# Kernel tuning notes

Hardware: AMD Instinct MI355X
Metric: run time of the kernel (lower is better)

Reference implementation:

```python
import jax, jax.numpy as jnp
import numpy as np

B, C, T = 8, 512, 8192
NQ, CBS, CBD = 9, 1024, 8
EPS = 1e-12  # F.normalize eps


def setup_inputs() -> dict:
    key = jax.random.key(0)
    ks = jax.random.split(key, 12)
    n = lambda i, shape, s: jax.random.normal(ks[i], shape, jnp.float32) * s
    return {
        "z": n(0, (B, C, T), 1.0),
        "down_w": n(1, (2, C, C, 2), 0.02),   # [layer, out, in, k] (torch Conv1d layout)
        "down_b": n(2, (2, C), 0.01),
        "up_w": n(3, (2, C, C, 2), 0.02),     # [layer, in, out, k] (torch ConvTranspose1d layout)
        "up_b": n(4, (2, C), 0.01),
        "in_v": n(5, (NQ, CBD, C), 0.05),     # weight_norm direction of in_proj 1x1 conv
        "in_g": 1.0 + n(6, (NQ, CBD), 0.02),  # weight_norm magnitude
        "in_b": n(7, (NQ, CBD), 0.01),
        "out_v": n(8, (NQ, C, CBD), 0.05),
        "out_g": 1.0 + n(9, (NQ, C), 0.02),
        "out_b": n(10, (NQ, C), 0.01),
        "codebooks": n(11, (NQ, CBS, CBD), 1.0),
    }


def _wn(g, v):
    # weight_norm (dim=0): per-output-row rescale
    return g[:, None] * v / jnp.linalg.norm(v, axis=1, keepdims=True)


def _l2norm(x):
    return x / jnp.maximum(jnp.linalg.norm(x, axis=-1, keepdims=True), EPS)


def _forward(z, down_w, down_b, up_w, up_b, in_v, in_g, in_b, out_v, out_g, out_b, codebooks):
    # --- downsample: two Conv1d(k=2, s=2) ---
    x = z
    for l in range(2):
        b, c, t = x.shape
        xr = x.reshape(b, c, t // 2, 2)
        x = jnp.einsum('bitk,oik->bot', xr, down_w[l]) + down_b[l][None, :, None]

    residual = x
    z_q = jnp.zeros_like(x)
    commit_loss = jnp.float32(0.0)
    cb_loss = jnp.float32(0.0)
    codes = []
    for i in range(NQ):
        # in_proj 1x1 conv (weight-normed)
        w_in = _wn(in_g[i], in_v[i])                 # [CBD, C]
        z_e = jnp.einsum('bdt,cd->bct', residual, w_in) + in_b[i][None, :, None]  # [B, CBD, T']
        # decode_latents: L2-normalize + squared-euclid via matmul + argmax
        bt = z_e.shape[0] * z_e.shape[2]
        enc = z_e.transpose(0, 2, 1).reshape(bt, CBD)
        enc_n = _l2norm(enc)
        cbk = codebooks[i]
        cb_n = _l2norm(cbk)
        dist = ((enc_n ** 2).sum(1, keepdims=True)
                - 2.0 * enc_n @ cb_n.T
                + (cb_n ** 2).sum(1)[None, :])        # [B*T', CBS]
        idx = jnp.argmax(-dist, axis=1).reshape(z_e.shape[0], -1)  # [B, T']
        z_q_i = cbk[idx].transpose(0, 2, 1)           # [B, CBD, T'] (un-normalized codebook rows)
        # losses (eval: mask all-true -> per-batch mean over (1,2) then batch mean == global mean)
        commit_loss = commit_loss + ((z_e - jax.lax.stop_gradient(z_q_i)) ** 2).mean()
        cb_loss = cb_loss + ((z_q_i - jax.lax.stop_gradient(z_e)) ** 2).mean()
        # straight-through + out_proj 1x1 conv (weight-normed)
        z_st = z_e + jax.lax.stop_gradient(z_q_i - z_e)
        w_out = _wn(out_g[i], out_v[i])               # [C, CBD]
        z_q_out = jnp.einsum('bct,dc->bdt', z_st, w_out) + out_b[i][None, :, None]
        z_q = z_q + z_q_out
        residual = residual - z_q_out
        codes.append(idx)
    codes = jnp.stack(codes, axis=1)                  # [B, NQ, T']

    x = z_q
    for l in range(2):
        b, c, t = x.shape
        x = jnp.einsum('bit,iok->botk', x, up_w[l]).reshape(b, C, t * 2) + up_b[l][None, :, None]
    return x, codes, commit_loss, cb_loss


def reference(z, down_w, down_b, up_w, up_b, in_v, in_g, in_b, out_v, out_g, out_b, codebooks):
    return _forward(z, down_w, down_b, up_w, up_b, in_v, in_g, in_b, out_v, out_g, out_b, codebooks)
```

## Files before the change

### kernel.cpp

```cpp
#include <hip/hip_runtime.h>
#include <math.h>


using u16 = unsigned short;
typedef __attribute__((ext_vector_type(8))) short bf16x8;
typedef __attribute__((ext_vector_type(8))) u16 su16x8;
typedef __attribute__((ext_vector_type(4))) float f32x4;

constexpr int NQ = 9, CBS = 1024, CBD = 8;
constexpr int TQ = 2048;
constexpr int NTOK = 16384;
constexpr int ASTR = 524288;
#define EPSN 1e-12f

constexpr size_t OFF_X1   = 0;
constexpr size_t OFF_U2   = 0;
constexpr size_t OFF_Q    = 14417920;
constexpr size_t OFF_E0T  = 15597568;
constexpr size_t OFF_X2   = 16777216;
constexpr size_t OFF_ZQF  = OFF_X2;
constexpr size_t OFF_DWP  = OFF_X2 + 8388608;
constexpr size_t OFF_UWP  = OFF_DWP + 1572864;
constexpr size_t OFF_WINN = OFF_UWP + 1048576;
constexpr size_t OFF_WOUT = OFF_WINN + 36864;
constexpr size_t OFF_CBS  = OFF_WOUT + 36864;
constexpr size_t OFF_PT   = OFF_CBS + 18432;
constexpr size_t OFF_BEFF = OFF_PT + 2340;
constexpr size_t OFF_BSUM = OFF_BEFF + 72;
constexpr size_t OFF_LOSS = OFF_BSUM + 512;

__global__ void prep_wp(const float* __restrict__ down_w, const float* __restrict__ up_w,
                        float* __restrict__ ws) {
  int idx = blockIdx.x * 256 + threadIdx.x;
  int mat = idx >> 19, e = idx & 524287;
  if (mat < 2) {
    float v = down_w[(size_t)mat * 524288 + e];
    u16* dst = (u16*)(ws + OFF_DWP) + (size_t)mat * 3 * ASTR;
    unsigned u = __float_as_uint(v);
    dst[e] = (u16)(u >> 16);
    float r = v - __uint_as_float(u & 0xFFFF0000u);
    unsigned ur = __float_as_uint(r);
    dst[ASTR + e] = (u16)(ur >> 16);
    float r2 = r - __uint_as_float(ur & 0xFFFF0000u);
    dst[2 * ASTR + e] = (u16)(__float_as_uint(r2) >> 16);
  } else {
    int l = mat - 2;
    int m = e >> 9, c = e & 511;
    float v = up_w[(size_t)l * 524288 + ((size_t)c * 512 + (m >> 1)) * 2 + (m & 1)];
    u16* dst = (u16*)(ws + OFF_UWP) + (size_t)l * 2 * ASTR;
    unsigned u = __float_as_uint(v);
    dst[e] = (u16)(u >> 16);
    float r = v - __uint_as_float(u & 0xFFFF0000u);
    dst[ASTR + e] = (u16)(__float_as_uint(r) >> 16);
  }
}

__global__ void prep_small1(const float* __restrict__ in_v, const float* __restrict__ in_g,
                            const float* __restrict__ out_v, const float* __restrict__ out_g,
                            const float* __restrict__ out_b, const float* __restrict__ codebooks,
                            float* __restrict__ ws) {
  int bid = blockIdx.x, tid = threadIdx.x;
  if (bid < 18) {
    int wid = bid * 4 + (tid >> 6), lane = tid & 63;
    if (wid < 72) {
      const float* v = in_v + (size_t)wid * 512;
      float ss = 0.f;
      for (int c = lane; c < 512; c += 64) ss += v[c] * v[c];
      #pragma unroll
      for (int o = 32; o; o >>= 1) ss += __shfl_xor(ss, o);
      float sc = in_g[wid] / sqrtf(ss);
      float* dst = ws + OFF_WINN + (size_t)wid * 512;
      for (int c = lane; c < 512; c += 64) dst[c] = v[c] * sc;
    }
  } else if (bid < 36) {
    int r = (bid - 18) * 256 + tid;
    if (r < 4608) {
      int i = r >> 9, c = r & 511;
      const float* v = out_v + (size_t)r * 8;
      float ss = 0.f;
      #pragma unroll
      for (int d = 0; d < 8; d++) ss += v[d] * v[d];
      float sc = out_g[r] / sqrtf(ss);
      float* dst = ws + OFF_WOUT + (size_t)c * 72 + i * 8;
      #pragma unroll
      for (int d = 0; d < 8; d++) dst[d] = v[d] * sc;
    }
  } else if (bid < 72) {
    int r = (bid - 36) * 256 + tid;
    if (r < 9216) {
      int i = r >> 10, j = r & 1023;
      const float* v = codebooks + (size_t)r * 8;
      float ss = 0.f;
      #pragma unroll
      for (int d = 0; d < 8; d++) ss += v[d] * v[d];
      float nm = fmaxf(sqrtf(ss), EPSN);
      float nsq = 0.f;
      #pragma unroll
      for (int d = 0; d < 8; d++) { float cn = v[d] / nm; nsq += cn * cn; }
      ws[OFF_CBS + ((size_t)i * 2 + 0) * 1024 + j] = 2.0f / nm;
      ws[OFF_CBS + ((size_t)i * 2 + 1) * 1024 + j] = nsq;
    }
  } else {
    int c = (bid - 72) * 256 + tid;
    if (c < 512) {
      float s = 0.f;
      #pragma unroll
      for (int j = 0; j < 9; j++) s += out_b[j * 512 + c];
      ws[OFF_BSUM + c] = s;
    }
  }
}

__global__ void prep2(const float* __restrict__ in_b, const float* __restrict__ out_b,
                      float* __restrict__ ws) {
  int gw = blockIdx.x * 4 + (threadIdx.x >> 6), lane = threadIdx.x & 63;
  const float* WinN = ws + OFF_WINN;
  const float* WoutS = ws + OFF_WOUT;
  if (gw < 2304) {
    int tri = gw >> 6, dd = gw & 63;
    int ip = 1;
    while (tri >= ip * (ip + 1) / 2) ip++;
    int i = tri - ip * (ip - 1) / 2;
    int d = dd >> 3, dp = dd & 7;
    const float* a = WinN + (size_t)(ip * 8 + d) * 512;
    float s = 0.f;
    for (int c = lane; c < 512; c += 64) s += a[c] * WoutS[(size_t)c * 72 + i * 8 + dp];
    #pragma unroll
    for (int o = 32; o; o >>= 1) s += __shfl_xor(s, o);
    if (lane == 0) ws[OFF_PT + (size_t)tri * 65 + dd] = s;
  } else if (gw < 2376) {
    int r = gw - 2304;
    int i = r >> 3;
    const float* a = WinN + (size_t)r * 512;
    float s = 0.f;
    for (int c = lane; c < 512; c += 64) {
      float ob = 0.f;
      for (int j = 0; j < i; j++) ob += out_b[j * 512 + c];
      s += a[c] * ob;
    }
    #pragma unroll
    for (int o = 32; o; o >>= 1) s += __shfl_xor(s, o);
    if (lane == 0) ws[OFF_BEFF + r] = in_b[r] - s;
  }
}

template <int NS, int GM, int EPI>
__global__ __launch_bounds__(256) void gemmT(const u16* __restrict__ Ap,
                                             const float* __restrict__ Bsrc,
                                             const float* __restrict__ bias,
                                             float* __restrict__ Out,
                                             int K, int N) {
  __shared__ u16 Bp[2][NS][128][32];
  const int tid = threadIdx.x;
  const int w = tid >> 6, l = tid & 63;
  const int g = l >> 4, li = l & 15;
  const int wr = w >> 1, wc = w & 1;
  const int n0 = blockIdx.x * 128, m0 = blockIdx.y * 128;
  const int nn = tid & 127, kw = tid >> 7;
  const int bb = (GM == 0) ? (n0 >> 12) : (n0 >> 11);
  const int tb = (GM == 0) ? ((n0 & 4095) + nn) : ((n0 & 2047) + nn);

  f32x4 acc[4][4];
  #pragma unroll
  for (int a = 0; a < 4; a++)
    #pragma unroll
    for (int b = 0; b < 4; b++) acc[a][b] = (f32x4){0.f, 0.f, 0.f, 0.f};

  float pvA[16], pvB[16];

#define LOADB(PV, K0)                                                           \
  if constexpr (GM == 0) {                                                      \
    int i0_ = ((K0) >> 1) + kw * 8;                                             \
    _Pragma("unroll")                                                           \
    for (int j2_ = 0; j2_ < 8; ++j2_)                                           \
      *(float2*)&PV[2 * j2_] =                                                  \
          *(const float2*)(Bsrc + ((size_t)(bb * 512 + i0_ + j2_) << 13) + 2 * tb); \
  } else if constexpr (GM == 1) {                                               \
    int i0_ = ((K0) >> 1) + kw * 8;                                             \
    _Pragma("unroll")                                                           \
    for (int j2_ = 0; j2_ < 8; ++j2_)                                           \
      *(float2*)&PV[2 * j2_] =                                                  \
          *(const float2*)(Bsrc + ((size_t)(i0_ + j2_) << 15) + bb * 4096 + 2 * tb); \
  } else {                                                                      \
    _Pragma("unroll")                                                           \
    for (int j_ = 0; j_ < 16; ++j_)                                             \
      PV[j_] = Bsrc[(size_t)((K0) + kw * 16 + j_) * N + n0 + nn];               \
  }

  const int sw = (nn >> 1) & 3;
  const int c0 = ((2 * kw) ^ sw) << 3, c1 = ((2 * kw + 1) ^ sw) << 3;

#define STAGE(BUF, PV)                                                          \
  {                                                                             \
    su16x8 pa_[NS], pb_[NS];                                                    \
    _Pragma("unroll")                                                           \
    for (int j_ = 0; j_ < 8; ++j_) {                                            \
      {                                                                         \
        float v_ = PV[j_];                                                      \
        unsigned u_ = __float_as_uint(v_);                                      \
        pa_[0][j_] = (u16)(u_ >> 16);                                           \
        float r_ = v_ - __uint_as_float(u_ & 0xFFFF0000u);                      \
        unsigned ur_ = __float_as_uint(r_);                                     \
        pa_[1][j_] = (u16)(ur_ >> 16);                                          \
        if constexpr (NS == 3) {                                                \
          float r2_ = r_ - __uint_as_float(ur_ & 0xFFFF0000u);                  \
          pa_[2][j_] = (u16)(__float_as_uint(r2_) >> 16);                       \
        }                                                                       \
      }                                                                         \
      {                                                                         \
        float v_ = PV[8 + j_];                                                  \
        unsigned u_ = __float_as_uint(v_);                                      \
        pb_[0][j_] = (u16)(u_ >> 16);                                           \
        float r_ = v_ - __uint_as_float(u_ & 0xFFFF0000u);                      \
        unsigned ur_ = __float_as_uint(r_);                                     \
        pb_[1][j_] = (u16)(ur_ >> 16);                                          \
        if constexpr (NS == 3) {                                                \
          float r2_ = r_ - __uint_as_float(ur_ & 0xFFFF0000u);                  \
          pb_[2][j_] = (u16)(__float_as_uint(r2_) >> 16);                       \
        }                                                                       \
      }                                                                         \
    }                                                                           \
    _Pragma("unroll")                                                           \
    for (int p_ = 0; p_ < NS; ++p_) {                                           \
      *(su16x8*)&Bp[BUF][p_][nn][c0] = pa_[p_];                                 \
      *(su16x8*)&Bp[BUF][p_][nn][c1] = pb_[p_];                                 \
    }                                                                           \
  }

#define COMPUTE(BUF, K0)                                                        \
  {                                                                             \
    bf16x8 bfr_[4][NS];                                                         \
    _Pragma("unroll")                                                           \
    for (int fn_ = 0; fn_ < 4; ++fn_) {                                         \
      int row_ = wc * 64 + fn_ * 16 + li;                                       \
      int cs_ = ((g ^ ((row_ >> 1) & 3)) << 3);                                 \
      _Pragma("unroll")                                                         \
      for (int q_ = 0; q_ < NS; ++q_)                                           \
        bfr_[fn_][q_] = *(const bf16x8*)&Bp[BUF][q_][row_][cs_];                \
    }                                                                           \
    const u16* arow_ = Ap + (size_t)(m0 + wr * 64 + li) * K + (K0) + g * 8;     \
    _Pragma("unroll")                                                           \
    for (int fm_ = 0; fm_ < 4; ++fm_) {                                         \
      bf16x8 afr_[NS];                                                          \
      _Pragma("unroll")                                                         \
      for (int p_ = 0; p_ < NS; ++p_)                                           \
        afr_[p_] = *(const bf16x8*)(arow_ + (size_t)p_ * ASTR + (size_t)fm_ * 16 * K); \
      _Pragma("unroll")                                                         \
      for (int fn_ = 0; fn_ < 4; ++fn_) {                                       \
        f32x4 a_ = acc[fm_][fn_];                                               \
        if constexpr (NS == 3) {                                                \
          a_ = __builtin_amdgcn_mfma_f32_16x16x32_bf16(afr_[2], bfr_[fn_][0], a_, 0, 0, 0); \
          a_ = __builtin_amdgcn_mfma_f32_16x16x32_bf16(afr_[1], bfr_[fn_][1], a_, 0, 0, 0); \
          a_ = __builtin_amdgcn_mfma_f32_16x16x32_bf16(afr_[0], bfr_[fn_][2], a_, 0, 0, 0); \
          a_ = __builtin_amdgcn_mfma_f32_16x16x32_bf16(afr_[1], bfr_[fn_][0], a_, 0, 0, 0); \
          a_ = __builtin_amdgcn_mfma_f32_16x16x32_bf16(afr_[0], bfr_[fn_][1], a_, 0, 0, 0); \
          a_ = __builtin_amdgcn_mfma_f32_16x16x32_bf16(afr_[0], bfr_[fn_][0], a_, 0, 0, 0); \
        } else {                                                                \
          a_ = __builtin_amdgcn_mfma_f32_16x16x32_bf16(afr_[1], bfr_[fn_][0], a_, 0, 0, 0); \
          a_ = __builtin_amdgcn_mfma_f32_16x16x32_bf16(afr_[0], bfr_[fn_][1], a_, 0, 0, 0); \
          a_ = __builtin_amdgcn_mfma_f32_16x16x32_bf16(afr_[0], bfr_[fn_][0], a_, 0, 0, 0); \
        }                                                                       \
        acc[fm_][fn_] = a_;                                                     \
      }                                                                         \
    }                                                                           \
  }

  LOADB(pvA, 0)
  LOADB(pvB, 32)
  STAGE(0, pvA)
  if (64 < K) { LOADB(pvA, 64) }
  __syncthreads();

  for (int k0 = 0; k0 < K; k0 += 64) {
    STAGE(1, pvB)
    if (k0 + 96 < K) { LOADB(pvB, k0 + 96) }
    COMPUTE(0, k0)
    __syncthreads();
    if (k0 + 64 < K) { STAGE(0, pvA) }
    if (k0 + 128 < K) { LOADB(pvA, k0 + 128) }
    COMPUTE(1, k0 + 32)
    __syncthreads();
  }
#undef LOADB
#undef STAGE
#undef COMPUTE

  const int mb = m0 + wr * 64 + g * 4;
  const int nb = n0 + wc * 64 + li;
  if constexpr (EPI == 0) {
    #pragma unroll
    for (int fn = 0; fn < 4; ++fn) {
      int n = nb + fn * 16;
      #pragma unroll
      for (int fm = 0; fm < 4; ++fm)
        #pragma unroll
        for (int r = 0; r < 4; ++r) {
          int o = mb + fm * 16 + r;
          Out[(size_t)o * 32768 + n] = acc[fm][fn][r] + bias[o];
        }
    }
  } else if constexpr (EPI == 1) {
    #pragma unroll
    for (int fn = 0; fn < 4; ++fn) {
      int n = nb + fn * 16;
      int b = n >> 11, t = n & 2047;
      #pragma unroll
      for (int fm = 0; fm < 4; ++fm)
        #pragma unroll
        for (int r = 0; r < 4; ++r) {
          int o = mb + fm * 16 + r;
          Out[((size_t)((b << 9) + o)) * 2048 + t] = acc[fm][fn][r] + bias[o];
        }
    }
  } else if constexpr (EPI == 2) {
    #pragma unroll
    for (int fn = 0; fn < 4; ++fn) {
      int n = nb + fn * 16;
      int b = n >> 11, t = n & 2047;
      #pragma unroll
      for (int fm = 0; fm < 4; ++fm)
        #pragma unroll
        for (int rp = 0; rp < 2; ++rp) {
          int m2 = mb + fm * 16 + 2 * rp;
          int o = m2 >> 1;
          float bv = bias[o];
          float2 st = make_float2(acc[fm][fn][2 * rp] + bv, acc[fm][fn][2 * rp + 1] + bv);
          *(float2*)&Out[(size_t)o * 32768 + (size_t)b * 4096 + 2 * t] = st;
        }
    }
  } else {
    #pragma unroll
    for (int fn = 0; fn < 4; ++fn) {
      int n = nb + fn * 16;
      int b = n >> 12, t1 = n & 4095;
      #pragma unroll
      for (int fm = 0; fm < 4; ++fm)
        #pragma unroll
        for (int rp = 0; rp < 2; ++rp) {
          int m2 = mb + fm * 16 + 2 * rp;
          int o = m2 >> 1;
          float bv = bias[o];
          float2 st = make_float2(acc[fm][fn][2 * rp] + bv, acc[fm][fn][2 * rp + 1] + bv);
          *(float2*)&Out[((size_t)((b << 9) + o)) * 8192 + 2 * t1] = st;
        }
    }
  }
}

template <int GATHER, int SCATTER>
__global__ __launch_bounds__(256) void gemm_conv(const float* __restrict__ A,
                                                 const float* __restrict__ Bsrc,
                                                 const float* __restrict__ bias,
                                                 float* __restrict__ Out,
                                                 int M, int K, int N, int Tt) {
  constexpr int BM = 128, BN = 128, BK = 16;
  __shared__ float As[BK][BM + 4];
  __shared__ float Bs[BK][BN + 4];
  int tid = threadIdx.x;
  int tx = tid & 15, ty = tid >> 4;
  int n0 = blockIdx.x * BN, m0 = blockIdx.y * BM;
  int b = n0 / Tt, t0 = n0 % Tt;
  float acc[8][8];
  #pragma unroll
  for (int i = 0; i < 8; i++)
    #pragma unroll
    for (int j = 0; j < 8; j++) acc[i][j] = 0.f;

  for (int k0 = 0; k0 < K; k0 += BK) {
    #pragma unroll
    for (int rep = 0; rep < 2; rep++) {
      int f = tid + rep * 256;
      int row = f >> 2, c4 = (f & 3) << 2;
      int m = m0 + row, k = k0 + c4;
      float4 v = make_float4(0.f, 0.f, 0.f, 0.f);
      if (m < M) {
        if (k + 3 < K) {
          v = *(const float4*)(A + (size_t)m * K + k);
        } else {
          float tmp[4] = {0.f, 0.f, 0.f, 0.f};
          for (int c = 0; c < 4; c++)
            if (k + c < K) tmp[c] = A[(size_t)m * K + k + c];
          v = make_float4(tmp[0], tmp[1], tmp[2], tmp[3]);
        }
      }
      As[c4 + 0][row] = v.x; As[c4 + 1][row] = v.y;
      As[c4 + 2][row] = v.z; As[c4 + 3][row] = v.w;
    }
    #pragma unroll
    for (int rep = 0; rep < 2; rep++) {
      int f = tid + rep * 256;
      int kk = f >> 5, n4 = (f & 31) << 2;
      int k = k0 + kk;
      float4 v = make_float4(0.f, 0.f, 0.f, 0.f);
      if (GATHER == 1) {
        v = *(const float4*)(Bsrc + ((size_t)(b * K + k)) * Tt + t0 + n4);
      } else {
        if (k < K) v = *(const float4*)(Bsrc + (size_t)k * N + n0 + n4);
      }
      *(float4*)&Bs[kk][n4] = v;
    }
    __syncthreads();
    #pragma unroll
    for (int kk = 0; kk < BK; kk++) {
      float a[8], bb[8];
      *(float4*)&a[0] = *(float4*)&As[kk][ty * 8];
      *(float4*)&a[4] = *(float4*)&As[kk][ty * 8 + 4];
      *(float4*)&bb[0] = *(float4*)&Bs[kk][tx * 8];
      *(float4*)&bb[4] = *(float4*)&Bs[kk][tx * 8 + 4];
      #pragma unroll
      for (int i = 0; i < 8; i++)
        #pragma unroll
        for (int j = 0; j < 8; j++) acc[i][j] = fmaf(a[i], bb[j], acc[i][j]);
    }
    __syncthreads();
  }
  if (SCATTER == 0) {
    #pragma unroll
    for (int i = 0; i < 8; i++) {
      int m = m0 + ty * 8 + i;
      if (m < M) {
        float bv = bias ? bias[m] : 0.f;
        float* p = Out + ((size_t)(b * M + m)) * Tt + t0 + tx * 8;
        *(float4*)p = make_float4(acc[i][0] + bv, acc[i][1] + bv, acc[i][2] + bv, acc[i][3] + bv);
        *(float4*)(p + 4) = make_float4(acc[i][4] + bv, acc[i][5] + bv, acc[i][6] + bv, acc[i][7] + bv);
      }
    }
  } else {
    #pragma unroll
    for (int j = 0; j < 8; j++) {
      int n = n0 + tx * 8 + j;
      int m = m0 + ty * 8;
      if (m < M) {
        float* p = Out + (size_t)n * M + m;
        if (m + 7 < M) {
          *(float4*)p = make_float4(acc[0][j], acc[1][j], acc[2][j], acc[3][j]);
          *(float4*)(p + 4) = make_float4(acc[4][j], acc[5][j], acc[6][j], acc[7][j]);
        } else {
          for (int i = 0; i < 8 && m + i < M; i++) p[i] = acc[i][j];
        }
      }
    }
  }
}

__global__ __launch_bounds__(256) void rvq_kernel(const float* __restrict__ codebooks,
                                                  const float* __restrict__ e0t,
                                                  const float* __restrict__ cbsW,
                                                  const float* __restrict__ ptW,
                                                  const float* __restrict__ beffW,
                                                  float* __restrict__ Qout,
                                                  float* __restrict__ codesOut,
                                                  float* __restrict__ lossPart) {
  __shared__ float cbv[8][1024];
  __shared__ float cbs2[2][1024];
  __shared__ float Pt[36 * 65];
  __shared__ float est[16][72];
  __shared__ float lred[4];
  int tid = threadIdx.x, wid = tid >> 6, lane = tid & 63;
  int nb0 = blockIdx.x * 16;
  for (int idx = tid; idx < 2340; idx += 256) Pt[idx] = ptW[idx];
  for (int idx = tid; idx < 16 * 72; idx += 256)
    est[idx / 72][idx % 72] = e0t[(size_t)nb0 * 72 + idx] + beffW[idx % 72];
  float lossLocal = 0.f;

  for (int i = 0; i < NQ; i++) {
    __syncthreads();
    const float* cbg = codebooks + (size_t)i * CBS * CBD;
    for (int lin = tid; lin < 2048; lin += 256) {
      int j = lin >> 1, half = (lin & 1) << 2;
      float4 v = *(const float4*)(cbg + (size_t)j * 8 + half);
      cbv[half + 0][j] = v.x; cbv[half + 1][j] = v.y;
      cbv[half + 2][j] = v.z; cbv[half + 3][j] = v.w;
    }
    for (int lin = tid; lin < 1024; lin += 256) {
      cbs2[0][lin] = cbsW[((size_t)i * 2 + 0) * 1024 + lin];
      cbs2[1][lin] = cbsW[((size_t)i * 2 + 1) * 1024 + lin];
    }
    __syncthreads();

    float ze[4][8], en[4][8];
    #pragma unroll
    for (int w = 0; w < 4; w++) {
      int tokl = wid * 4 + w;
      float ss = 0.f;
      #pragma unroll
      for (int d = 0; d < 8; d++) { float v = est[tokl][i * 8 + d]; ze[w][d] = v; ss += v * v; }
      float inv = 1.0f / fmaxf(sqrtf(ss), EPSN);
      #pragma unroll
      for (int d = 0; d < 8; d++) en[w][d] = ze[w][d] * inv;
    }
    float best[4]; int bidx[4];
    #pragma unroll
    for (int w = 0; w < 4; w++) { best[w] = -INFINITY; bidx[w] = 0; }
    #pragma unroll 4
    for (int r = 0; r < 16; r++) {
      int j = lane + (r << 6);
      float c0 = cbv[0][j], c1 = cbv[1][j], c2 = cbv[2][j], c3 = cbv[3][j];
      float c4 = cbv[4][j], c5 = cbv[5][j], c6 = cbv[6][j], c7 = cbv[7][j];
      float ti = cbs2[0][j], ns = cbs2[1][j];
      #pragma unroll
      for (int w = 0; w < 4; w++) {
        float dt = en[w][0] * c0;
        dt = fmaf(en[w][1], c1, dt); dt = fmaf(en[w][2], c2, dt);
        dt = fmaf(en[w][3], c3, dt); dt = fmaf(en[w][4], c4, dt);
        dt = fmaf(en[w][5], c5, dt); dt = fmaf(en[w][6], c6, dt);
        dt = fmaf(en[w][7], c7, dt);
        float s = fmaf(dt, ti, -ns);
        if (s > best[w]) { best[w] = s; bidx[w] = j; }
      }
    }
    #pragma unroll
    for (int w = 0; w < 4; w++) {
      #pragma unroll
      for (int off = 32; off; off >>= 1) {
        float so = __shfl_xor(best[w], off);
        int jo = __shfl_xor(bidx[w], off);
        if (so > best[w] || (so == best[w] && jo < bidx[w])) { best[w] = so; bidx[w] = jo; }
      }
    }
    int d = lane & 7;
    #pragma unroll
    for (int w = 0; w < 4; w++) {
      int jstar = bidx[w];
      int tokl = wid * 4 + w;
      int n = nb0 + tokl;
      float qd = cbv[d][jstar];
      float diff = ze[w][d] - qd;
      float sq = diff * diff;
      sq += __shfl_xor(sq, 1); sq += __shfl_xor(sq, 2); sq += __shfl_xor(sq, 4);
      if (lane == 0) lossLocal += sq;
      if (lane < 8) Qout[(size_t)(i * 8 + lane) * NTOK + n] = qd;
      if (lane == 0) codesOut[(size_t)((n >> 11) * NQ + i) * TQ + (n & (TQ - 1))] = (float)jstar;
      if (i < NQ - 1) {
        int f = lane >> 3, d2 = lane & 7;
        int ip = i + 1 + f;
        if (ip < NQ) {
          int tri = (ip * (ip - 1)) / 2 + i;
          const float* prow = &Pt[tri * 65 + d2 * 8];
          float s = 0.f;
          #pragma unroll
          for (int dp = 0; dp < 8; dp++) s = fmaf(prow[dp], cbv[dp][jstar], s);
          est[tokl][ip * 8 + d2] -= s;
        }
      }
    }
  }
  if (lane == 0) lred[wid] = lossLocal;
  __syncthreads();
  if (tid == 0) {
    float s = ((lred[0] + lred[1]) + lred[2]) + lred[3];
    lossPart[blockIdx.x] = s;
  }
}

__global__ void loss_fin(const float* __restrict__ lossPart, float* __restrict__ out) {
  __shared__ float s[256];
  int tid = threadIdx.x;
  float v = 0.f;
  for (int r = 0; r < 4; r++) v += lossPart[tid + r * 256];
  s[tid] = v;
  __syncthreads();
  for (int w = 128; w; w >>= 1) {
    if (tid < w) s[tid] += s[tid + w];
    __syncthreads();
  }
  if (tid == 0) {
    float total = s[0] / 131072.0f;
    out[0] = total;
    out[1] = total;
  }
}

extern "C" void kernel_launch(void* const* d_in, const int* in_sizes, int n_in,
                              void* d_out, int out_size, void* d_ws, size_t ws_size,
                              hipStream_t stream) {
  const float* z      = (const float*)d_in[0];
  const float* down_w = (const float*)d_in[1];
  const float* down_b = (const float*)d_in[2];
  const float* up_w   = (const float*)d_in[3];
  const float* up_b   = (const float*)d_in[4];
  const float* in_v   = (const float*)d_in[5];
  const float* in_g   = (const float*)d_in[6];
  const float* in_b   = (const float*)d_in[7];
  const float* out_v  = (const float*)d_in[8];
  const float* out_g  = (const float*)d_in[9];
  const float* out_b  = (const float*)d_in[10];
  const float* codebooks = (const float*)d_in[11];
  float* ws = (float*)d_ws;
  float* xout = (float*)d_out;
  float* codesOut = xout + (size_t)8 * 512 * 8192;
  float* lossOut = codesOut + (size_t)8 * NQ * TQ;
  const u16* dwp = (const u16*)(ws + OFF_DWP);
  const u16* uwp = (const u16*)(ws + OFF_UWP);

  hipLaunchKernelGGL(prep_wp, dim3(8192), dim3(256), 0, stream, down_w, up_w, ws);
  hipLaunchKernelGGL(prep_small1, dim3(74), dim3(256), 0, stream,
                     in_v, in_g, out_v, out_g, out_b, codebooks, ws);
  hipLaunchKernelGGL(prep2, dim3(594), dim3(256), 0, stream, in_b, out_b, ws);
  hipLaunchKernelGGL((gemmT<3, 0, 0>), dim3(256, 4), dim3(256), 0, stream,
                     dwp, z, down_b, ws + OFF_X1, 1024, 32768);
  hipLaunchKernelGGL((gemmT<3, 1, 1>), dim3(128, 4), dim3(256), 0, stream,
                     dwp + (size_t)3 * ASTR, ws + OFF_X1, down_b + 512, ws + OFF_X2, 1024, 16384);
  hipLaunchKernelGGL((gemm_conv<1, 1>), dim3(128, 1), dim3(256), 0, stream,
                     ws + OFF_WINN, ws + OFF_X2, (const float*)nullptr, ws + OFF_E0T, 72, 512, 16384, 2048);
  hipLaunchKernelGGL(rvq_kernel, dim3(1024), dim3(256), 0, stream,
                     codebooks, ws + OFF_E0T, ws + OFF_CBS, ws + OFF_PT, ws + OFF_BEFF,
                     ws + OFF_Q, codesOut, ws + OFF_LOSS);
  hipLaunchKernelGGL((gemm_conv<2, 0>), dim3(128, 4), dim3(256), 0, stream,
                     ws + OFF_WOUT, ws + OFF_Q, ws + OFF_BSUM, ws + OFF_ZQF, 512, 72, 16384, 16384);
  hipLaunchKernelGGL((gemmT<2, 2, 2>), dim3(128, 8), dim3(256), 0, stream,
                     uwp, ws + OFF_ZQF, up_b, ws + OFF_U2, 512, 16384);
  hipLaunchKernelGGL((gemmT<2, 2, 3>), dim3(256, 8), dim3(256), 0, stream,
                     uwp + (size_t)2 * ASTR, ws + OFF_U2, up_b + 512, xout, 512, 32768);
  hipLaunchKernelGGL(loss_fin, dim3(1), dim3(256), 0, stream, ws + OFF_LOSS, lossOut);
}
```

Measured before the change: 965.9 us.

## Compose linear conv stages into single effective weight matrices

Because the two stride-2 downsample convolutions are linear with no activation between them, their weights are multiplied in advance into one 512x2048 stride-4 matrix, so z feeds one GEMM and the x1 intermediate disappears. On the output side, out_proj, both transposed convolutions and the bias sums are folded into a 2048x73 matrix applied straight to the 72-channel quantized codes. This removes the large intermediate writes and reads and two big GEMMs. In exchange it adds small weight-composition kernels on every call, and FP32 rounding differs from the staged computation.

Measured after the change: 860.7 us. 1.12x faster.

```diff
diff --git a/kernel.cpp b/kernel.cpp
--- a/kernel.cpp
+++ b/kernel.cpp
@@ -10,58 +10,36 @@
 constexpr int NQ = 9, CBS = 1024, CBD = 8;
 constexpr int TQ = 2048;
 constexpr int NTOK = 16384;
-constexpr int ASTR = 524288;
+constexpr int APS = 1048576;
 #define EPSN 1e-12f
 
-constexpr size_t OFF_X1   = 0;
-constexpr size_t OFF_U2   = 0;
-constexpr size_t OFF_Q    = 14417920;
-constexpr size_t OFF_E0T  = 15597568;
-constexpr size_t OFF_X2   = 16777216;
-constexpr size_t OFF_ZQF  = OFF_X2;
-constexpr size_t OFF_DWP  = OFF_X2 + 8388608;
-constexpr size_t OFF_UWP  = OFF_DWP + 1572864;
-constexpr size_t OFF_WINN = OFF_UWP + 1048576;
-constexpr size_t OFF_WOUT = OFF_WINN + 36864;
-constexpr size_t OFF_CBS  = OFF_WOUT + 36864;
-constexpr size_t OFF_PT   = OFF_CBS + 18432;
-constexpr size_t OFF_BEFF = OFF_PT + 2340;
-constexpr size_t OFF_BSUM = OFF_BEFF + 72;
-constexpr size_t OFF_LOSS = OFF_BSUM + 512;
-
-__global__ void prep_wp(const float* __restrict__ down_w, const float* __restrict__ up_w,
-                        float* __restrict__ ws) {
-  int idx = blockIdx.x * 256 + threadIdx.x;
-  int mat = idx >> 19, e = idx & 524287;
-  if (mat < 2) {
-    float v = down_w[(size_t)mat * 524288 + e];
-    u16* dst = (u16*)(ws + OFF_DWP) + (size_t)mat * 3 * ASTR;
-    unsigned u = __float_as_uint(v);
-    dst[e] = (u16)(u >> 16);
-    float r = v - __uint_as_float(u & 0xFFFF0000u);
-    unsigned ur = __float_as_uint(r);
-    dst[ASTR + e] = (u16)(ur >> 16);
-    float r2 = r - __uint_as_float(ur & 0xFFFF0000u);
-    dst[2 * ASTR + e] = (u16)(__float_as_uint(r2) >> 16);
-  } else {
-    int l = mat - 2;
-    int m = e >> 9, c = e & 511;
-    float v = up_w[(size_t)l * 524288 + ((size_t)c * 512 + (m >> 1)) * 2 + (m & 1)];
-    u16* dst = (u16*)(ws + OFF_UWP) + (size_t)l * 2 * ASTR;
-    unsigned u = __float_as_uint(v);
-    dst[e] = (u16)(u >> 16);
-    float r = v - __uint_as_float(u & 0xFFFF0000u);
-    dst[ASTR + e] = (u16)(__float_as_uint(r) >> 16);
-  }
-}
+constexpr size_t OFF_X2    = 0;
+constexpr size_t OFF_E0T   = 8388608;
+constexpr size_t OFF_Q     = 9568256;
+constexpr size_t OFF_WD    = 10747904;
+constexpr size_t OFF_WDP   = 11796480;
+constexpr size_t OFF_WEFF  = 13369344;
+constexpr size_t OFF_WX    = 14417920;
+constexpr size_t OFF_WINN  = 14581760;
+constexpr size_t OFF_WOUTS = 14618624;
+constexpr size_t OFF_CBS   = 14659584;
+constexpr size_t OFF_PT    = 14678016;
+constexpr size_t OFF_BEFF  = 14680356;
+constexpr size_t OFF_BSUM  = 14680428;
+constexpr size_t OFF_BD    = 14680940;
+constexpr size_t OFF_BUP   = 14681452;
+constexpr size_t OFF_LOSS  = 14682476;
 
 __global__ void prep_small1(const float* __restrict__ in_v, const float* __restrict__ in_g,
                             const float* __restrict__ out_v, const float* __restrict__ out_g,
                             const float* __restrict__ out_b, const float* __restrict__ codebooks,
+                            const float* __restrict__ down_w, const float* __restrict__ down_b,
+                            const float* __restrict__ up_w, const float* __restrict__ up_b,
                             float* __restrict__ ws) {
   int bid = blockIdx.x, tid = threadIdx.x;
+  int wid4 = tid >> 6, lane = tid & 63;
   if (bid < 18) {
-    int wid = bid * 4 + (tid >> 6), lane = tid & 63;
+    int wid = bid * 4 + wid4;
     if (wid < 72) {
       const float* v = in_v + (size_t)wid * 512;
       float ss = 0.f;
@@ -81,7 +59,7 @@
       #pragma unroll
       for (int d = 0; d < 8; d++) ss += v[d] * v[d];
       float sc = out_g[r] / sqrtf(ss);
-      float* dst = ws + OFF_WOUT + (size_t)c * 72 + i * 8;
+      float* dst = ws + OFF_WOUTS + (size_t)c * 80 + i * 8;
       #pragma unroll
       for (int d = 0; d < 8; d++) dst[d] = v[d] * sc;
     }
@@ -100,14 +78,37 @@
       ws[OFF_CBS + ((size_t)i * 2 + 0) * 1024 + j] = 2.0f / nm;
       ws[OFF_CBS + ((size_t)i * 2 + 1) * 1024 + j] = nsq;
     }
-  } else {
+  } else if (bid < 74) {
     int c = (bid - 72) * 256 + tid;
     if (c < 512) {
       float s = 0.f;
       #pragma unroll
       for (int j = 0; j < 9; j++) s += out_b[j * 512 + c];
       ws[OFF_BSUM + c] = s;
-    }
+      ws[OFF_WOUTS + (size_t)c * 80 + 72] = s;
+      #pragma unroll
+      for (int d = 73; d < 80; d++) ws[OFF_WOUTS + (size_t)c * 80 + d] = 0.f;
+    }
+  } else if (bid < 202) {
+    int o = (bid - 74) * 4 + wid4;
+    float s = 0.f;
+    for (int m = lane; m < 512; m += 64) {
+      float w0 = down_w[524288 + (size_t)o * 1024 + m * 2];
+      float w1 = down_w[524288 + (size_t)o * 1024 + m * 2 + 1];
+      s += (w0 + w1) * down_b[m];
+    }
+    #pragma unroll
+    for (int off = 32; off; off >>= 1) s += __shfl_xor(s, off);
+    if (lane == 0) ws[OFF_BD + o] = s + down_b[512 + o];
+  } else {
+    int gw = (bid - 202) * 4 + wid4;
+    int c = gw >> 1, j2 = gw & 1;
+    float s = 0.f;
+    for (int m = lane; m < 512; m += 64)
+      s += up_w[524288 + (size_t)m * 1024 + c * 2 + j2] * up_b[m];
+    #pragma unroll
+    for (int off = 32; off; off >>= 1) s += __shfl_xor(s, off);
+    if (lane == 0) ws[OFF_BUP + gw] = s + up_b[512 + c];
   }
 }
 
@@ -115,7 +116,7 @@
                       float* __restrict__ ws) {
   int gw = blockIdx.x * 4 + (threadIdx.x >> 6), lane = threadIdx.x & 63;
   const float* WinN = ws + OFF_WINN;
-  const float* WoutS = ws + OFF_WOUT;
+  const float* WoutS = ws + OFF_WOUTS;
   if (gw < 2304) {
     int tri = gw >> 6, dd = gw & 63;
     int ip = 1;
@@ -124,7 +125,7 @@
     int d = dd >> 3, dp = dd & 7;
     const float* a = WinN + (size_t)(ip * 8 + d) * 512;
     float s = 0.f;
-    for (int c = lane; c < 512; c += 64) s += a[c] * WoutS[(size_t)c * 72 + i * 8 + dp];
+    for (int c = lane; c < 512; c += 64) s += a[c] * WoutS[(size_t)c * 80 + i * 8 + dp];
     #pragma unroll
     for (int o = 32; o; o >>= 1) s += __shfl_xor(s, o);
     if (lane == 0) ws[OFF_PT + (size_t)tri * 65 + dd] = s;
@@ -144,12 +145,121 @@
   }
 }
 
-template <int NS, int GM, int EPI>
-__global__ __launch_bounds__(256) void gemmT(const u16* __restrict__ Ap,
-                                             const float* __restrict__ Bsrc,
-                                             const float* __restrict__ bias,
-                                             float* __restrict__ Out,
-                                             int K, int N) {
+template <int WHICH>
+__global__ __launch_bounds__(256) void smallmm(const float* __restrict__ src,
+                                               float* __restrict__ outp) {
+  __shared__ float As[32][68];
+  __shared__ float Bs[32][68];
+  const int tid = threadIdx.x;
+  const int tx = tid & 15, ty = tid >> 4;
+  const int b0 = blockIdx.x * 64, a0 = blockIdx.y * 64, j = blockIdx.z;
+  const int jh = j >> 1, jl = j & 1;
+  float acc[4][4];
+  #pragma unroll
+  for (int i = 0; i < 4; i++)
+    #pragma unroll
+    for (int k = 0; k < 4; k++) acc[i][k] = 0.f;
+
+  for (int k0 = 0; k0 < 512; k0 += 32) {
+    #pragma unroll
+    for (int rep = 0; rep < 8; rep++) {
+      int f = tid + rep * 256;
+      int aa = f >> 5, mm = f & 31;
+      size_t ai;
+      if constexpr (WHICH == 0) ai = 524288 + (size_t)(a0 + aa) * 1024 + (k0 + mm) * 2 + jh;
+      else                      ai = 524288 + (size_t)(k0 + mm) * 1024 + (a0 + aa) * 2 + jl;
+      As[mm][aa] = src[ai];
+      int mm2 = f >> 6, bb = f & 63;
+      size_t bi;
+      if constexpr (WHICH == 0) bi = (size_t)(k0 + mm2) * 1024 + (b0 + bb) * 2 + jl;
+      else                      bi = (size_t)(b0 + bb) * 1024 + (k0 + mm2) * 2 + jh;
+      Bs[mm2][bb] = src[bi];
+    }
+    __syncthreads();
+    #pragma unroll
+    for (int kk = 0; kk < 32; kk++) {
+      float av[4], bv[4];
+      #pragma unroll
+      for (int i = 0; i < 4; i++) av[i] = As[kk][ty * 4 + i];
+      #pragma unroll
+      for (int i = 0; i < 4; i++) bv[i] = Bs[kk][tx * 4 + i];
+      #pragma unroll
+      for (int i = 0; i < 4; i++)
+        #pragma unroll
+        for (int k = 0; k < 4; k++) acc[i][k] = fmaf(av[i], bv[k], acc[i][k]);
+    }
+    __syncthreads();
+  }
+  #pragma unroll
+  for (int i = 0; i < 4; i++) {
+    int a = a0 + ty * 4 + i;
+    #pragma unroll
+    for (int k = 0; k < 4; k++) {
+      int b = b0 + tx * 4 + k;
+      if constexpr (WHICH == 0) outp[(size_t)a * 2048 + b * 4 + j] = acc[i][k];
+      else                      outp[((size_t)a * 4 + j) * 512 + b] = acc[i][k];
+    }
+  }
+}
+
+__global__ void prep_wdsplit(const float* __restrict__ wd, u16* __restrict__ wdp) {
+  int idx = blockIdx.x * 256 + threadIdx.x;
+  float v = wd[idx];
+  unsigned u = __float_as_uint(v);
+  wdp[idx] = (u16)(u >> 16);
+  float r = v - __uint_as_float(u & 0xFFFF0000u);
+  unsigned ur = __float_as_uint(r);
+  wdp[APS + idx] = (u16)(ur >> 16);
+  float r2 = r - __uint_as_float(ur & 0xFFFF0000u);
+  wdp[2 * APS + idx] = (u16)(__float_as_uint(r2) >> 16);
+}
+
+__global__ __launch_bounds__(256) void prep_wx(const float* __restrict__ weff,
+                                               const float* __restrict__ wouts,
+                                               float* __restrict__ wx) {
+  __shared__ float Wes[16][512];
+  __shared__ float WSs[64][80];
+  const int tid = threadIdx.x;
+  const int m0 = blockIdx.x * 16;
+  #pragma unroll
+  for (int rep = 0; rep < 32; rep++) {
+    int f = tid + rep * 256;
+    Wes[f >> 9][f & 511] = weff[(size_t)(m0 + (f >> 9)) * 512 + (f & 511)];
+  }
+  const int rowq = tid >> 4, rq = tid & 15;
+  float accs[5] = {0.f, 0.f, 0.f, 0.f, 0.f};
+  for (int k0 = 0; k0 < 512; k0 += 64) {
+    __syncthreads();
+    #pragma unroll
+    for (int rep = 0; rep < 20; rep++) {
+      int f = tid + rep * 256;
+      int kk = f / 80, col = f % 80;
+      WSs[kk][col] = wouts[(size_t)(k0 + kk) * 80 + col];
+    }
+    __syncthreads();
+    #pragma unroll 4
+    for (int kk = 0; kk < 64; kk++) {
+      float we = Wes[rowq][k0 + kk];
+      #pragma unroll
+      for (int s = 0; s < 5; s++) accs[s] = fmaf(we, WSs[kk][rq + 16 * s], accs[s]);
+    }
+  }
+  #pragma unroll
+  for (int s = 0; s < 5; s++) {
+    int r = rq + 16 * s;
+    if (r < 73) wx[(size_t)(m0 + rowq) * 80 + r] = accs[s];
+  }
+  if (tid < 112) {
+    int row = tid / 7, col = 73 + tid % 7;
+    wx[(size_t)(m0 + row) * 80 + col] = 0.f;
+  }
+}
+
+__global__ __launch_bounds__(256) void gemm_down(const u16* __restrict__ Ap,
+                                                 const float* __restrict__ z,
+                                                 const float* __restrict__ bias,
+                                                 float* __restrict__ Out) {
+  constexpr int NS = 3, K = 2048;
   __shared__ u16 Bp[2][NS][128][32];
   const int tid = threadIdx.x;
   const int w = tid >> 6, l = tid & 63;
@@ -157,8 +267,8 @@
   const int wr = w >> 1, wc = w & 1;
   const int n0 = blockIdx.x * 128, m0 = blockIdx.y * 128;
   const int nn = tid & 127, kw = tid >> 7;
-  const int bb = (GM == 0) ? (n0 >> 12) : (n0 >> 11);
-  const int tb = (GM == 0) ? ((n0 & 4095) + nn) : ((n0 & 2047) + nn);
+  const int bb = n0 >> 11;
+  const int tb = (n0 & 2047) + nn;
 
   f32x4 acc[4][4];
   #pragma unroll
@@ -169,22 +279,12 @@
   float pvA[16], pvB[16];
 
 #define LOADB(PV, K0)                                                           \
-  if constexpr (GM == 0) {                                                      \
-    int i0_ = ((K0) >> 1) + kw * 8;                                             \
+  {                                                                             \
+    int c0_ = ((K0) >> 2) + kw * 4;                                             \
     _Pragma("unroll")                                                           \
-    for (int j2_ = 0; j2_ < 8; ++j2_)                                           \
-      *(float2*)&PV[2 * j2_] =                                                  \
-          *(const float2*)(Bsrc + ((size_t)(bb * 512 + i0_ + j2_) << 13) + 2 * tb); \
-  } else if constexpr (GM == 1) {                                               \
-    int i0_ = ((K0) >> 1) + kw * 8;                                             \
-    _Pragma("unroll")                                                           \
-    for (int j2_ = 0; j2_ < 8; ++j2_)                                           \
-      *(float2*)&PV[2 * j2_] =                                                  \
-          *(const float2*)(Bsrc + ((size_t)(i0_ + j2_) << 15) + bb * 4096 + 2 * tb); \
-  } else {                                                                      \
-    _Pragma("unroll")                                                           \
-    for (int j_ = 0; j_ < 16; ++j_)                                             \
-      PV[j_] = Bsrc[(size_t)((K0) + kw * 16 + j_) * N + n0 + nn];               \
+    for (int cc_ = 0; cc_ < 4; ++cc_)                                           \
+      *(float4*)&PV[4 * cc_] =                                                  \
+          *(const float4*)(z + ((size_t)(bb * 512 + c0_ + cc_) << 13) + 4 * tb);\
   }
 
   const int sw = (nn >> 1) & 3;
@@ -202,10 +302,8 @@
         float r_ = v_ - __uint_as_float(u_ & 0xFFFF0000u);                      \
         unsigned ur_ = __float_as_uint(r_);                                     \
         pa_[1][j_] = (u16)(ur_ >> 16);                                          \
-        if constexpr (NS == 3) {                                                \
-          float r2_ = r_ - __uint_as_float(ur_ & 0xFFFF0000u);                  \
-          pa_[2][j_] = (u16)(__float_as_uint(r2_) >> 16);                       \
-        }                                                                       \
+        float r2_ = r_ - __uint_as_float(ur_ & 0xFFFF0000u);                    \
+        pa_[2][j_] = (u16)(__float_as_uint(r2_) >> 16);                         \
       }                                                                         \
       {                                                                         \
         float v_ = PV[8 + j_];                                                  \
@@ -214,10 +312,8 @@
         float r_ = v_ - __uint_as_float(u_ & 0xFFFF0000u);                      \
         unsigned ur_ = __float_as_uint(r_);                                     \
         pb_[1][j_] = (u16)(ur_ >> 16);                                          \
-        if constexpr (NS == 3) {                                                \
-          float r2_ = r_ - __uint_as_float(ur_ & 0xFFFF0000u);                  \
-          pb_[2][j_] = (u16)(__float_as_uint(r2_) >> 16);                       \
-        }                                                                       \
+        float r2_ = r_ - __uint_as_float(ur_ & 0xFFFF0000u);                    \
+        pb_[2][j_] = (u16)(__float_as_uint(r2_) >> 16);                         \
       }                                                                         \
     }                                                                           \
     _Pragma("unroll")                                                           \
@@ -244,23 +340,17 @@
       bf16x8 afr_[NS];                                                          \
       _Pragma("unroll")                                                         \
       for (int p_ = 0; p_ < NS; ++p_)                                           \
-        afr_[p_] = *(const bf16x8*)(arow_ + (size_t)p_ * ASTR + (size_t)fm_ * 16 * K); \
+        afr_[p_] = *(const bf16x8*)(arow_ + (size_t)p_ * APS + (size_t)fm_ * 16 * K); \
       _Pragma("unroll")                                                         \
       for (int fn_ = 0; fn_ < 4; ++fn_) {                                       \
         f32x4 a_ = acc[fm_][fn_];                                               \
-        if constexpr (NS == 3) {                                                \
-          a_ = __builtin_amdgcn_mfma_f32_16x16x32_bf16(afr_[2], bfr_[fn_][0], a_, 0, 0, 0); \
-          a_ = __builtin_amdgcn_mfma_f32_16x16x32_bf16(afr_[1], bfr_[fn_][1], a_, 0, 0, 0); \
-          a_ = __builtin_amdgcn_mfma_f32_16x16x32_bf16(afr_[0], bfr_[fn_][2], a_, 0, 0, 0); \
-          a_ = __builtin_amdgcn_mfma_f32_16x16x32_bf16(afr_[1], bfr_[fn_][0], a_, 0, 0, 0); \
-          a_ = __builtin_amdgcn_mfma_f32_16x16x32_bf16(afr_[0], bfr_[fn_][1], a_, 0, 0, 0); \
-          a_ = __builtin_amdgcn_mfma_f32_16x16x32_bf16(afr_[0], bfr_[fn_][0], a_, 0, 0, 0); \
-        } else {                                                                \
-          a_ = __builtin_amdgcn_mfma_f32_16x16x32_bf16(afr_[1], bfr_[fn_][0], a_, 0, 0, 0); \
-          a_ = __builtin_amdgcn_mfma_f32_16x16x32_bf16(afr_[0], bfr_[fn_][1], a_, 0, 0, 0); \
-          a_ = __builtin_amdgcn_mfma_f32_16x16x32_bf16(afr_[0], bfr_[fn_][0], a_, 0, 0, 0); \
-        }                                                                       \
-        acc[fm_][fn_] = a_;                                                     \
+        a_ = __builtin_amdgcn_mfma_f32_16x16x32_bf16(afr_[2], bfr_[fn_][0], a_, 0, 0, 0); \
+        a_ = __builtin_amdgcn_mfma_f32_16x16x32_bf16(afr_[1], bfr_[fn_][1], a_, 0, 0, 0); \
+        a_ = __builtin_amdgcn_mfma_f32_16x16x32_bf16(afr_[0], bfr_[fn_][2], a_, 0, 0, 0); \
+        a_ = __builtin_amdgcn_mfma_f32_16x16x32_bf16(afr_[1], bfr_[fn_][0], a_, 0, 0, 0); \
+        a_ = __builtin_amdgcn_mfma_f32_16x16x32_bf16(afr_[0], bfr_[fn_][1], a_, 0, 0, 0); \
+        a_ = __builtin_amdgcn_mfma_f32_16x16x32_bf16(afr_[0], bfr_[fn_][0], a_, 0, 0, 0); \
+      acc[fm_][fn_] = a_;                                                       \
       }                                                                         \
     }                                                                           \
   }
@@ -268,7 +358,7 @@
   LOADB(pvA, 0)
   LOADB(pvB, 32)
   STAGE(0, pvA)
-  if (64 < K) { LOADB(pvA, 64) }
+  LOADB(pvA, 64)
   __syncthreads();
 
   for (int k0 = 0; k0 < K; k0 += 64) {
@@ -287,63 +377,17 @@
 
   const int mb = m0 + wr * 64 + g * 4;
   const int nb = n0 + wc * 64 + li;
-  if constexpr (EPI == 0) {
-    #pragma unroll
-    for (int fn = 0; fn < 4; ++fn) {
-      int n = nb + fn * 16;
-      #pragma unroll
-      for (int fm = 0; fm < 4; ++fm)
-        #pragma unroll
-        for (int r = 0; r < 4; ++r) {
-          int o = mb + fm * 16 + r;
-          Out[(size_t)o * 32768 + n] = acc[fm][fn][r] + bias[o];
-        }
-    }
-  } else if constexpr (EPI == 1) {
-    #pragma unroll
-    for (int fn = 0; fn < 4; ++fn) {
-      int n = nb + fn * 16;
-      int b = n >> 11, t = n & 2047;
-      #pragma unroll
-      for (int fm = 0; fm < 4; ++fm)
-        #pragma unroll
-        for (int r = 0; r < 4; ++r) {
-          int o = mb + fm * 16 + r;
-          Out[((size_t)((b << 9) + o)) * 2048 + t] = acc[fm][fn][r] + bias[o];
-        }
-    }
-  } else if constexpr (EPI == 2) {
-    #pragma unroll
-    for (int fn = 0; fn < 4; ++fn) {
-      int n = nb + fn * 16;
-      int b = n >> 11, t = n & 2047;
-      #pragma unroll
-      for (int fm = 0; fm < 4; ++fm)
-        #pragma unroll
-        for (int rp = 0; rp < 2; ++rp) {
-          int m2 = mb + fm * 16 + 2 * rp;
-          int o = m2 >> 1;
-          float bv = bias[o];
-          float2 st = make_float2(acc[fm][fn][2 * rp] + bv, acc[fm][fn][2 * rp + 1] + bv);
-          *(float2*)&Out[(size_t)o * 32768 + (size_t)b * 4096 + 2 * t] = st;
-        }
-    }
-  } else {
-    #pragma unroll
-    for (int fn = 0; fn < 4; ++fn) {
-      int n = nb + fn * 16;
-      int b = n >> 12, t1 = n & 4095;
-      #pragma unroll
-      for (int fm = 0; fm < 4; ++fm)
-        #pragma unroll
-        for (int rp = 0; rp < 2; ++rp) {
-          int m2 = mb + fm * 16 + 2 * rp;
-          int o = m2 >> 1;
-          float bv = bias[o];
-          float2 st = make_float2(acc[fm][fn][2 * rp] + bv, acc[fm][fn][2 * rp + 1] + bv);
-          *(float2*)&Out[((size_t)((b << 9) + o)) * 8192 + 2 * t1] = st;
-        }
-    }
+  #pragma unroll
+  for (int fn = 0; fn < 4; ++fn) {
+    int n = nb + fn * 16;
+    int b = n >> 11, t = n & 2047;
+    #pragma unroll
+    for (int fm = 0; fm < 4; ++fm)
+      #pragma unroll
+      for (int r = 0; r < 4; ++r) {
+        int o = mb + fm * 16 + r;
+        Out[((size_t)((b << 9) + o)) * 2048 + t] = acc[fm][fn][r] + bias[o];
+      }
   }
 }
 
@@ -439,6 +483,74 @@
           for (int i = 0; i < 8 && m + i < M; i++) p[i] = acc[i][j];
         }
       }
+    }
+  }
+}
+
+__global__ __launch_bounds__(256) void xfin(const float* __restrict__ wx,
+                                            const float* __restrict__ Q,
+                                            const float* __restrict__ bup,
+                                            float* __restrict__ xout) {
+  __shared__ float Wxs[128][80];
+  __shared__ float Qs[128][80];
+  const int tid = threadIdx.x;
+  const int n0 = blockIdx.x * 128, m0 = blockIdx.y * 128;
+  #pragma unroll
+  for (int rep = 0; rep < 10; rep++) {
+    int f = tid + rep * 256;
+    *(float4*)&Wxs[0][f * 4] = *(const float4*)(wx + (size_t)m0 * 80 + f * 4);
+  }
+  {
+    int nn = tid & 127, r0 = tid >> 7;
+    for (int r = r0; r < 72; r += 2)
+      Qs[nn][r] = Q[(size_t)r * 16384 + n0 + nn];
+  }
+  __syncthreads();
+
+  const int txn = tid & 15, tym = tid >> 4;
+  float acc[8][8];
+  #pragma unroll
+  for (int i = 0; i < 8; i++)
+    #pragma unroll
+    for (int j = 0; j < 8; j++) acc[i][j] = 0.f;
+
+  #pragma unroll 2
+  for (int r4 = 0; r4 < 18; r4++) {
+    float4 wv[8], qv[8];
+    #pragma unroll
+    for (int i = 0; i < 8; i++) wv[i] = *(const float4*)&Wxs[tym * 8 + i][r4 * 4];
+    #pragma unroll
+    for (int j = 0; j < 8; j++) qv[j] = *(const float4*)&Qs[txn * 8 + j][r4 * 4];
+    #pragma unroll
+    for (int i = 0; i < 8; i++)
+      #pragma unroll
+      for (int j = 0; j < 8; j++) {
+        acc[i][j] = fmaf(wv[i].x, qv[j].x, acc[i][j]);
+        acc[i][j] = fmaf(wv[i].y, qv[j].y, acc[i][j]);
+        acc[i][j] = fmaf(wv[i].z, qv[j].z, acc[i][j]);
+        acc[i][j] = fmaf(wv[i].w, qv[j].w, acc[i][j]);
+      }
+  }
+
+  float bxv[8];
+  #pragma unroll
+  for (int mi = 0; mi < 8; mi++) {
+    int mp = m0 + tym * 8 + mi;
+    bxv[mi] = Wxs[tym * 8 + mi][72] + bup[(mp >> 2) * 2 + (mp & 1)];
+  }
+  #pragma unroll
+  for (int cg = 0; cg < 2; cg++) {
+    int mp0 = m0 + tym * 8 + cg * 4;
+    int c = mp0 >> 2;
+    #pragma unroll
+    for (int j = 0; j < 8; j++) {
+      int n = n0 + txn * 8 + j;
+      int b = n >> 11, t = n & 2047;
+      float4 sv = make_float4(acc[cg * 4 + 0][j] + bxv[cg * 4 + 0],
+                              acc[cg * 4 + 1][j] + bxv[cg * 4 + 1],
+                              acc[cg * 4 + 2][j] + bxv[cg * 4 + 2],
+                              acc[cg * 4 + 3][j] + bxv[cg * 4 + 3]);
+      *(float4*)&xout[((size_t)((b << 9) + c)) * 8192 + 4 * t] = sv;
     }
   }
 }
@@ -590,27 +702,25 @@
   float* xout = (float*)d_out;
   float* codesOut = xout + (size_t)8 * 512 * 8192;
   float* lossOut = codesOut + (size_t)8 * NQ * TQ;
-  const u16* dwp = (const u16*)(ws + OFF_DWP);
-  const u16* uwp = (const u16*)(ws + OFF_UWP);
-
-  hipLaunchKernelGGL(prep_wp, dim3(8192), dim3(256), 0, stream, down_w, up_w, ws);
-  hipLaunchKernelGGL(prep_small1, dim3(74), dim3(256), 0, stream,
-                     in_v, in_g, out_v, out_g, out_b, codebooks, ws);
+
+  hipLaunchKernelGGL(prep_small1, dim3(458), dim3(256), 0, stream,
+                     in_v, in_g, out_v, out_g, out_b, codebooks,
+                     down_w, down_b, up_w, up_b, ws);
   hipLaunchKernelGGL(prep2, dim3(594), dim3(256), 0, stream, in_b, out_b, ws);
-  hipLaunchKernelGGL((gemmT<3, 0, 0>), dim3(256, 4), dim3(256), 0, stream,
-                     dwp, z, down_b, ws + OFF_X1, 1024, 32768);
-  hipLaunchKernelGGL((gemmT<3, 1, 1>), dim3(128, 4), dim3(256), 0, stream,
-                     dwp + (size_t)3 * ASTR, ws + OFF_X1, down_b + 512, ws + OFF_X2, 1024, 16384);
+  hipLaunchKernelGGL((smallmm<0>), dim3(8, 8, 4), dim3(256), 0, stream, down_w, ws + OFF_WD);
+  hipLaunchKernelGGL((smallmm<1>), dim3(8, 8, 4), dim3(256), 0, stream, up_w, ws + OFF_WEFF);
+  hipLaunchKernelGGL(prep_wdsplit, dim3(4096), dim3(256), 0, stream,
+                     ws + OFF_WD, (u16*)(ws + OFF_WDP));
+  hipLaunchKernelGGL(prep_wx, dim3(128), dim3(256), 0, stream,
+                     ws + OFF_WEFF, ws + OFF_WOUTS, ws + OFF_WX);
+  hipLaunchKernelGGL(gemm_down, dim3(128, 4), dim3(256), 0, stream,
+                     (const u16*)(ws + OFF_WDP), z, ws + OFF_BD, ws + OFF_X2);
   hipLaunchKernelGGL((gemm_conv<1, 1>), dim3(128, 1), dim3(256), 0, stream,
                      ws + OFF_WINN, ws + OFF_X2, (const float*)nullptr, ws + OFF_E0T, 72, 512, 16384, 2048);
   hipLaunchKernelGGL(rvq_kernel, dim3(1024), dim3(256), 0, stream,
                      codebooks, ws + OFF_E0T, ws + OFF_CBS, ws + OFF_PT, ws + OFF_BEFF,
                      ws + OFF_Q, codesOut, ws + OFF_LOSS);
-  hipLaunchKernelGGL((gemm_conv<2, 0>), dim3(128, 4), dim3(256), 0, stream,
-                     ws + OFF_WOUT, ws + OFF_Q, ws + OFF_BSUM, ws + OFF_ZQF, 512, 72, 16384, 16384);
-  hipLaunchKernelGGL((gemmT<2, 2, 2>), dim3(128, 8), dim3(256), 0, stream,
-                     uwp, ws + OFF_ZQF, up_b, ws + OFF_U2, 512, 16384);
-  hipLaunchKernelGGL((gemmT<2, 2, 3>), dim3(256, 8), dim3(256), 0, stream,
-                     uwp + (size_t)2 * ASTR, ws + OFF_U2, up_b + 512, xout, 512, 32768);
+  hipLaunchKernelGGL(xfin, dim3(128, 16), dim3(256), 0, stream,
+                     ws + OFF_WX, ws + OFF_Q, ws + OFF_BUP, xout);
   hipLaunchKernelGGL(loss_fin, dim3(1), dim3(256), 0, stream, ws + OFF_LOSS, lossOut);
 }
```
